# Kernel tuning notes

Measured on AMD Instinct MI355X. Metric: run time of the kernel, lower is better.

Reference implementation:

```python
import jax, jax.numpy as jnp
import numpy as np

E = 1024      # embed_size
H = 16        # heads
D = E // H    # head_dim = 64
FF = 4 * E    # forward_expansion * embed_size
B = 2
S = 2048
LN_EPS = 1e-5


def setup_inputs() -> dict:
    key = jax.random.key(0)
    ks = jax.random.split(key, 16)
    sc = 0.02
    inp = {
        'value': jax.random.normal(ks[0], (B, S, E), jnp.float32),
        'key':   jax.random.normal(ks[1], (B, S, E), jnp.float32),
        'query': jax.random.normal(ks[2], (B, S, E), jnp.float32),
        # causal mask, broadcast over batch and heads; 0 => masked
        'mask': jnp.tril(jnp.ones((S, S), jnp.int32))[None, None],
        # fc_out: Linear(E, E)
        'Wo': jax.random.normal(ks[3], (E, E), jnp.float32) * sc,
        'bo': jnp.zeros((E,), jnp.float32),
        # pH gate: Linear(E, E)
        'Wg': jax.random.normal(ks[4], (E, E), jnp.float32) * sc,
        'bg': jnp.zeros((E,), jnp.float32),
        # LayerNorms
        'g1': jnp.ones((E,), jnp.float32), 'b1': jnp.zeros((E,), jnp.float32),
        'g2': jnp.ones((E,), jnp.float32), 'b2': jnp.zeros((E,), jnp.float32),
        # FFN
        'W1': jax.random.normal(ks[5], (E, FF), jnp.float32) * sc,
        'bf1': jnp.zeros((FF,), jnp.float32),
        'W2': jax.random.normal(ks[6], (FF, E), jnp.float32) * sc,
        'bf2': jnp.zeros((E,), jnp.float32),
    }
    return inp


def layer_norm(x, g, b):
    mu = jnp.mean(x, axis=-1, keepdims=True)
    var = jnp.mean(jnp.square(x - mu), axis=-1, keepdims=True)
    return (x - mu) * jax.lax.rsqrt(var + LN_EPS) * g + b


def reference(value, key, query, mask, Wo, bo, Wg, bg, g1, b1, g2, b2, W1, bf1, W2, bf2):
    N, seq_len, _ = query.shape
    # NOTE: original module defines per-head Linear(values/keys/queries) but never
    # applies them in forward; faithful reference omits them too.
    v = value.reshape(N, seq_len, H, D).transpose(0, 2, 1, 3)  # nhkd
    k = key.reshape(N, seq_len, H, D).transpose(0, 2, 1, 3)
    q = query.reshape(N, seq_len, H, D).transpose(0, 2, 1, 3)  # nhqd

    energy = jnp.einsum('nhqd,nhkd->nhqk', q, k)
    energy = jnp.where(mask == 0, jnp.float32(-1e20), energy)
    # faithful: mask applied BEFORE scaling by 1/sqrt(head_dim)
    attention = jax.nn.softmax(energy / jnp.sqrt(jnp.float32(D)), axis=-1)
    out = jnp.einsum('nhqk,nhkd->nhqd', attention, v)
    out = out.transpose(0, 2, 1, 3).reshape(N, seq_len, E)
    attn_output = out @ Wo + bo

    x_avg = jnp.mean(query, axis=1, keepdims=True)       # (N,1,E)
    gate = jax.nn.sigmoid(x_avg @ Wg + bg)               # (N,1,E)
    gated = gate * attn_output

    x = layer_norm(gated + query, g1, b1)                # dropout p=0 -> identity
    ff = jax.nn.gelu(x @ W1 + bf1, approximate=False) @ W2 + bf2
    out_final = layer_norm(ff + x, g2, b2)
    return out_final
```

## Files before the change

kernel.cpp:

```cpp
#include <hip/hip_runtime.h>
#include <hip/hip_bf16.h>

#define S_LEN 2048
#define EMB   1024
#define NH    16
#define HD    64
#define FF_DIM 4096
#define BATCH 2

typedef __attribute__((ext_vector_type(8))) short bf16x8;
typedef __attribute__((ext_vector_type(4))) float f32x4;

__device__ __forceinline__ short f2bf(float x) {
  __hip_bfloat16 h = (__hip_bfloat16)x;
  return *(short*)&h;
}
__device__ __forceinline__ bf16x8 pack8(float4 a, float4 b) {
  bf16x8 o;
  o[0] = f2bf(a.x); o[1] = f2bf(a.y); o[2] = f2bf(a.z); o[3] = f2bf(a.w);
  o[4] = f2bf(b.x); o[5] = f2bf(b.y); o[6] = f2bf(b.z); o[7] = f2bf(b.w);
  return o;
}

__device__ __forceinline__ void gl2lds16(const void* g, void* l) {
  __builtin_amdgcn_global_load_lds(
      (const __attribute__((address_space(1))) unsigned*)g,
      (__attribute__((address_space(3))) unsigned*)l, 16, 0, 0);
}

__device__ __forceinline__ void transpose_tile(
    const float* in, short* outS, int R, int C, int bx, int by, int t) {
  __shared__ short Ts[64][65];
  int cb = bx * 64, rb = by * 64;
  for (int idx = t; idx < 4096; idx += 256) {
    int r = idx >> 6, c = idx & 63;
    Ts[r][c] = f2bf(in[(size_t)(rb + r) * C + cb + c]);
  }
  __syncthreads();
  for (int idx = t; idx < 4096; idx += 256) {
    int oc = idx >> 6, orr = idx & 63;
    outS[(size_t)(cb + oc) * R + rb + orr] = Ts[orr][oc];
  }
}

__global__ __launch_bounds__(256) void transpose_all(
    const float* __restrict__ Wo, const float* __restrict__ W1,
    const float* __restrict__ W2, __hip_bfloat16* __restrict__ WoT,
    __hip_bfloat16* __restrict__ W1T, __hip_bfloat16* __restrict__ W2T) {
  int id = blockIdx.x, t = threadIdx.x;
  if (id < 256)        transpose_tile(Wo, (short*)WoT, EMB, EMB,    id & 15,          id >> 4,          t);
  else if (id < 1280)  transpose_tile(W1, (short*)W1T, EMB, FF_DIM, (id - 256) & 63,  (id - 256) >> 6,  t);
  else                 transpose_tile(W2, (short*)W2T, FF_DIM, EMB, (id - 1280) & 15, (id - 1280) >> 4, t);
}

__global__ __launch_bounds__(256) void zero_f32(float* __restrict__ p) {
  p[blockIdx.x * 256 + threadIdx.x] = 0.f;
}

__global__ __launch_bounds__(256) void xavg_partial(
    const float* __restrict__ Q, float* __restrict__ xavg) {
  int b = blockIdx.y;
  int s0 = blockIdx.x * 16;
  int t = threadIdx.x;
  const float* base = Q + ((size_t)b * S_LEN + s0) * EMB + 4 * t;
  float4 acc = {0.f, 0.f, 0.f, 0.f};
#pragma unroll 4
  for (int r = 0; r < 16; r++) {
    float4 v = *(const float4*)(base + (size_t)r * EMB);
    acc.x += v.x; acc.y += v.y; acc.z += v.z; acc.w += v.w;
  }
  float* dst = xavg + b * EMB + 4 * t;
  const float inv = 1.f / (float)S_LEN;
  atomicAdd(dst + 0, acc.x * inv);
  atomicAdd(dst + 1, acc.y * inv);
  atomicAdd(dst + 2, acc.z * inv);
  atomicAdd(dst + 3, acc.w * inv);
}

__global__ __launch_bounds__(256) void gate_kernel(
    const float* __restrict__ xavg, const float* __restrict__ Wg,
    const float* __restrict__ bg, float* __restrict__ gate) {
  __shared__ float red[4][64];
  int b = blockIdx.y;
  int nl = threadIdx.x & 63;
  int n = blockIdx.x * 64 + nl;
  int kg = threadIdx.x >> 6;
  const float* xa = xavg + b * EMB;
  float s = 0.f;
#pragma unroll 4
  for (int k = kg * 256; k < kg * 256 + 256; k++)
    s += xa[k] * Wg[(size_t)k * EMB + n];
  red[kg][nl] = s;
  __syncthreads();
  if (kg == 0) {
    float tot = red[0][nl] + red[1][nl] + red[2][nl] + red[3][nl] + bg[n];
    gate[b * EMB + n] = 1.f / (1.f + __expf(-tot));
  }
}

__global__ __launch_bounds__(256) void pack_kv(
    const float* __restrict__ Kg, const float* __restrict__ Vg,
    __hip_bfloat16* __restrict__ Kp, __hip_bfloat16* __restrict__ Vt) {
  __shared__ short Vs[64][72];
  int s0 = blockIdx.x * 64, h = blockIdx.y, b = blockIdx.z;
  int t = threadIdx.x, r = t >> 2, c = (t & 3) * 16;
  size_t gin = ((size_t)b * S_LEN + s0 + r) * EMB + h * HD + c;
  {
    float4 a0 = *(const float4*)(Kg + gin);
    float4 a1 = *(const float4*)(Kg + gin + 4);
    float4 a2 = *(const float4*)(Kg + gin + 8);
    float4 a3 = *(const float4*)(Kg + gin + 12);
    short* kp = (short*)Kp + (((size_t)b * NH + h) * S_LEN + s0 + r) * HD + c;
    *(bf16x8*)(kp)     = pack8(a0, a1);
    *(bf16x8*)(kp + 8) = pack8(a2, a3);
  }
  {
    float4 a0 = *(const float4*)(Vg + gin);
    float4 a1 = *(const float4*)(Vg + gin + 4);
    float4 a2 = *(const float4*)(Vg + gin + 8);
    float4 a3 = *(const float4*)(Vg + gin + 12);
    *(bf16x8*)&Vs[r][c]     = pack8(a0, a1);
    *(bf16x8*)&Vs[r][c + 8] = pack8(a2, a3);
  }
  __syncthreads();
  bf16x8 o0, o1;
#pragma unroll
  for (int j = 0; j < 8; j++) o0[j] = Vs[c + j][r];
#pragma unroll
  for (int j = 0; j < 8; j++) o1[j] = Vs[c + 8 + j][r];
  short* vp = (short*)Vt + (((size_t)b * NH + h) * HD + r) * S_LEN + s0 + c;
  *(bf16x8*)(vp)     = o0;
  *(bf16x8*)(vp + 8) = o1;
}

__global__ __launch_bounds__(256) void flash_attn_mfma(
    const float* __restrict__ Q, const __hip_bfloat16* __restrict__ Kp,
    const __hip_bfloat16* __restrict__ Vtb, __hip_bfloat16* __restrict__ O) {
  __shared__ short Ks[64][72];
  __shared__ short Vt[64][72];
  __shared__ short Ps[4][16][72];
  int t = threadIdx.x;
  int w = t >> 6, lane = t & 63, quad = lane >> 4, l15 = lane & 15;
  int j = blockIdx.x;
  int p = j & 255, g = j >> 8;
  int bh = p & 31, c_ = p >> 5;
  int qb = (g == 0) ? c_ : (g == 1) ? (15 - c_) : (g == 2) ? (16 + c_) : (31 - c_);
  int h = bh & 15, b = bh >> 4;
  size_t base = ((size_t)b * S_LEN) * EMB + h * HD;
  const short* kpb = (const short*)Kp + ((size_t)b * NH + h) * S_LEN * HD;
  const short* vtb = (const short*)Vtb + ((size_t)b * NH + h) * HD * S_LEN;

  bf16x8 qf[2];
  {
    const float* qrow = Q + base + (size_t)(qb * 64 + w * 16 + l15) * EMB;
#pragma unroll
    for (int kc = 0; kc < 2; kc++) {
      float4 a = *(const float4*)(qrow + kc * 32 + quad * 8);
      float4 c = *(const float4*)(qrow + kc * 32 + quad * 8 + 4);
      a.x *= 0.125f; a.y *= 0.125f; a.z *= 0.125f; a.w *= 0.125f;
      c.x *= 0.125f; c.y *= 0.125f; c.z *= 0.125f; c.w *= 0.125f;
      qf[kc] = pack8(a, c);
    }
  }

  f32x4 acc[4];
  float lsum[4];
  f32x4 zero = {0.f, 0.f, 0.f, 0.f};
#pragma unroll
  for (int n = 0; n < 4; n++) acc[n] = zero;
#pragma unroll
  for (int r = 0; r < 4; r++) lsum[r] = 0.f;

  int r0 = t >> 2, c0 = (t & 3) * 16;
  bf16x8 kf0, kf1, vf0, vf1;
  {
    const short* kr = kpb + (size_t)r0 * HD + c0;
    kf0 = *(const bf16x8*)(kr); kf1 = *(const bf16x8*)(kr + 8);
    const short* vr = vtb + (size_t)r0 * S_LEN + c0;
    vf0 = *(const bf16x8*)(vr); vf1 = *(const bf16x8*)(vr + 8);
  }

  for (int kt = 0; kt <= qb; kt++) {
    __syncthreads();
    *(bf16x8*)&Ks[r0][c0]     = kf0;
    *(bf16x8*)&Ks[r0][c0 + 8] = kf1;
    *(bf16x8*)&Vt[r0][c0]     = vf0;
    *(bf16x8*)&Vt[r0][c0 + 8] = vf1;
    __syncthreads();
    if (kt < qb) {
      const short* kr = kpb + (size_t)((kt + 1) * 64 + r0) * HD + c0;
      kf0 = *(const bf16x8*)(kr); kf1 = *(const bf16x8*)(kr + 8);
      const short* vr = vtb + (size_t)r0 * S_LEN + (kt + 1) * 64 + c0;
      vf0 = *(const bf16x8*)(vr); vf1 = *(const bf16x8*)(vr + 8);
    }

    f32x4 sc[4];
#pragma unroll
    for (int n = 0; n < 4; n++) sc[n] = zero;
#pragma unroll
    for (int n = 0; n < 4; n++)
#pragma unroll
      for (int kc = 0; kc < 2; kc++) {
        bf16x8 kf = *(const bf16x8*)&Ks[n * 16 + l15][kc * 32 + quad * 8];
        sc[n] = __builtin_amdgcn_mfma_f32_16x16x32_bf16(qf[kc], kf, sc[n], 0, 0, 0);
      }

    bool diag = (kt == qb);
#pragma unroll
    for (int r = 0; r < 4; r++) {
      float p0 = __expf(sc[0][r]);
      float p1 = __expf(sc[1][r]);
      float p2 = __expf(sc[2][r]);
      float p3 = __expf(sc[3][r]);
      if (diag) {
        int rowL = w * 16 + quad * 4 + r;
        if (l15      > rowL) p0 = 0.f;
        if (l15 + 16 > rowL) p1 = 0.f;
        if (l15 + 32 > rowL) p2 = 0.f;
        if (l15 + 48 > rowL) p3 = 0.f;
      }
      lsum[r] += (p0 + p1) + (p2 + p3);
      short* prow = &Ps[w][quad * 4 + r][l15];
      prow[0]  = f2bf(p0);
      prow[16] = f2bf(p1);
      prow[32] = f2bf(p2);
      prow[48] = f2bf(p3);
    }
    asm volatile("s_waitcnt lgkmcnt(0)" ::: "memory");

    bf16x8 pf0 = *(const bf16x8*)&Ps[w][l15][quad * 8];
    bf16x8 pf1 = *(const bf16x8*)&Ps[w][l15][32 + quad * 8];
#pragma unroll
    for (int n = 0; n < 4; n++) {
      bf16x8 vfa = *(const bf16x8*)&Vt[n * 16 + l15][quad * 8];
      acc[n] = __builtin_amdgcn_mfma_f32_16x16x32_bf16(pf0, vfa, acc[n], 0, 0, 0);
      bf16x8 vfb = *(const bf16x8*)&Vt[n * 16 + l15][32 + quad * 8];
      acc[n] = __builtin_amdgcn_mfma_f32_16x16x32_bf16(pf1, vfb, acc[n], 0, 0, 0);
    }
  }

#pragma unroll
  for (int r = 0; r < 4; r++) {
    float l = lsum[r];
#pragma unroll
    for (int off = 1; off < 16; off <<= 1) l += __shfl_xor(l, off);
    float invl = 1.f / l;
    size_t orow = base + (size_t)(qb * 64 + w * 16 + quad * 4 + r) * EMB;
#pragma unroll
    for (int n = 0; n < 4; n++)
      O[orow + n * 16 + l15] = (__hip_bfloat16)(acc[n][r] * invl);
  }
}

template <int MODE, int TM>
__global__ __launch_bounds__(256) void gemm_bt(
    const __hip_bfloat16* __restrict__ A, const __hip_bfloat16* __restrict__ BT,
    int K, int N, const float* __restrict__ bias,
    const float* __restrict__ gate, const float* __restrict__ residF,
    const __hip_bfloat16* __restrict__ residB,
    float* __restrict__ outF, __hip_bfloat16* __restrict__ outB) {
  constexpr int MI = TM / 32;
  __shared__ short As[TM][32];
  __shared__ short Bs[128][32];
  int t = threadIdx.x;
  int w = t >> 6, lane = t & 63, quad = lane >> 4, l15 = lane & 15;
  int wm = (w >> 1) * (TM / 2), wn = (w & 1) * 64;
  int mBase = blockIdx.y * TM, nBase = blockIdx.x * 128;
  f32x4 acc[MI][4];
  f32x4 zero = {0.f, 0.f, 0.f, 0.f};
#pragma unroll
  for (int i = 0; i < MI; i++)
#pragma unroll
    for (int j = 0; j < 4; j++) acc[i][j] = zero;
  const short* Ag = (const short*)A;
  const short* Bg = (const short*)BT;
  int w16 = w * 16;
  int lr = lane >> 2;
  int lc = (lane & 3) * 8;
  for (int kb = 0; kb < K; kb += 32) {
    gl2lds16(&Ag[(size_t)(mBase + w16 + lr) * K + kb + lc], &As[w16][0]);
    if (TM == 128)
      gl2lds16(&Ag[(size_t)(mBase + 64 + w16 + lr) * K + kb + lc], &As[64 + w16][0]);
    gl2lds16(&Bg[(size_t)(nBase + w16 + lr) * K + kb + lc],      &Bs[w16][0]);
    gl2lds16(&Bg[(size_t)(nBase + 64 + w16 + lr) * K + kb + lc], &Bs[64 + w16][0]);
    __syncthreads();
    bf16x8 af[MI], bfr[4];
#pragma unroll
    for (int mi = 0; mi < MI; mi++) af[mi] = *(const bf16x8*)&As[wm + mi * 16 + l15][quad * 8];
#pragma unroll
    for (int ni = 0; ni < 4; ni++) bfr[ni] = *(const bf16x8*)&Bs[wn + ni * 16 + l15][quad * 8];
#pragma unroll
    for (int mi = 0; mi < MI; mi++)
#pragma unroll
      for (int ni = 0; ni < 4; ni++)
        acc[mi][ni] = __builtin_amdgcn_mfma_f32_16x16x32_bf16(af[mi], bfr[ni], acc[mi][ni], 0, 0, 0);
    __syncthreads();
  }
#pragma unroll
  for (int mi = 0; mi < MI; mi++) {
#pragma unroll
    for (int r = 0; r < 4; r++) {
      int row = mBase + wm + mi * 16 + quad * 4 + r;
#pragma unroll
      for (int ni = 0; ni < 4; ni++) {
        int col = nBase + wn + ni * 16 + l15;
        float v = acc[mi][ni][r];
        if (MODE == 0) {
          float g = gate[(row >> 11) * EMB + col];
          v = g * (v + bias[col]) + residF[(size_t)row * N + col];
          outF[(size_t)row * N + col] = v;
        } else if (MODE == 1) {
          v += bias[col];
          v = 0.5f * v * (1.0f + erff(v * 0.70710678118654752f));
          outB[(size_t)row * N + col] = (__hip_bfloat16)v;
        } else {
          v += bias[col] + (float)residB[(size_t)row * N + col];
          outF[(size_t)row * N + col] = v;
        }
      }
    }
  }
}

__device__ __forceinline__ float block_sum_256(float v) {
  __shared__ float sb[4];
#pragma unroll
  for (int off = 32; off > 0; off >>= 1) v += __shfl_down(v, off);
  int w = threadIdx.x >> 6, ln = threadIdx.x & 63;
  if (ln == 0) sb[w] = v;
  __syncthreads();
  float r = sb[0] + sb[1] + sb[2] + sb[3];
  __syncthreads();
  return r;
}

template <bool TO_BF16>
__global__ __launch_bounds__(256) void ln_kernel(
    const float* __restrict__ y, const float* __restrict__ g,
    const float* __restrict__ b, __hip_bfloat16* __restrict__ outB,
    float* __restrict__ outF) {
  size_t row = blockIdx.x;
  const float* yr = y + row * EMB;
  float v[4];
#pragma unroll
  for (int i = 0; i < 4; i++) v[i] = yr[threadIdx.x + i * 256];
  float s = block_sum_256(v[0] + v[1] + v[2] + v[3]);
  float mu = s * (1.f / (float)EMB);
  float q = 0.f;
#pragma unroll
  for (int i = 0; i < 4; i++) { float d = v[i] - mu; q += d * d; }
  q = block_sum_256(q);
  float rs = rsqrtf(q * (1.f / (float)EMB) + 1e-5f);
#pragma unroll
  for (int i = 0; i < 4; i++) {
    int e = threadIdx.x + i * 256;
    float o = (v[i] - mu) * rs * g[e] + b[e];
    if (TO_BF16) outB[row * EMB + e] = (__hip_bfloat16)o;
    else         outF[row * EMB + e] = o;
  }
}

extern "C" void kernel_launch(void* const* d_in, const int* in_sizes, int n_in,
                              void* d_out, int out_size, void* d_ws, size_t ws_size,
                              hipStream_t stream) {
  const float* Val = (const float*)d_in[0];
  const float* Key = (const float*)d_in[1];
  const float* Qry = (const float*)d_in[2];
  const float* Wo  = (const float*)d_in[4];
  const float* bo  = (const float*)d_in[5];
  const float* Wg  = (const float*)d_in[6];
  const float* bg  = (const float*)d_in[7];
  const float* g1  = (const float*)d_in[8];
  const float* b1  = (const float*)d_in[9];
  const float* g2  = (const float*)d_in[10];
  const float* b2  = (const float*)d_in[11];
  const float* W1  = (const float*)d_in[12];
  const float* bf1 = (const float*)d_in[13];
  const float* W2  = (const float*)d_in[14];
  const float* bf2 = (const float*)d_in[15];
  float* out = (float*)d_out;

  char* ws = (char*)d_ws;
  size_t off = 0;
  auto alloc = [&](size_t bytes) {
    char* p = ws + off;
    off += (bytes + 255) & ~(size_t)255;
    return p;
  };
  const size_t MB = 1024 * 1024;
  bool bigws = ws_size >= 78 * MB;

  __hip_bfloat16* WoT = (__hip_bfloat16*)alloc((size_t)EMB * EMB * 2);
  __hip_bfloat16* W1T = (__hip_bfloat16*)alloc((size_t)EMB * FF_DIM * 2);
  __hip_bfloat16* W2T = (__hip_bfloat16*)alloc((size_t)EMB * FF_DIM * 2);
  size_t kvRegion = bigws ? (size_t)BATCH * S_LEN * FF_DIM * 2
                          : (size_t)S_LEN * FF_DIM * 2;
  char* kvBase = alloc(kvRegion);
  __hip_bfloat16* Kpk  = (__hip_bfloat16*)kvBase;
  __hip_bfloat16* Vtb  = (__hip_bfloat16*)(kvBase + 8 * MB);
  __hip_bfloat16* Hbuf = (__hip_bfloat16*)kvBase;
  __hip_bfloat16* attnO = (__hip_bfloat16*)alloc((size_t)BATCH * S_LEN * EMB * 2);
  float* ybuf = (float*)alloc((size_t)BATCH * S_LEN * EMB * 4);
  float* xavg = (float*)alloc(BATCH * EMB * 4);
  float* gate = (float*)alloc(BATCH * EMB * 4);
  __hip_bfloat16* xb = attnO;
  float* zbuf = ybuf;

  transpose_all<<<2304, 256, 0, stream>>>(Wo, W1, W2, WoT, W1T, W2T);
  zero_f32<<<BATCH * EMB / 256, 256, 0, stream>>>(xavg);
  xavg_partial<<<dim3(128, BATCH), 256, 0, stream>>>(Qry, xavg);
  gate_kernel<<<dim3(16, BATCH), 256, 0, stream>>>(xavg, Wg, bg, gate);
  pack_kv<<<dim3(32, NH, BATCH), 256, 0, stream>>>(Key, Val, Kpk, Vtb);
  flash_attn_mfma<<<1024, 256, 0, stream>>>(Qry, Kpk, Vtb, attnO);
  gemm_bt<0, 64><<<dim3(8, 64), 256, 0, stream>>>(attnO, WoT, EMB, EMB, bo, gate, Qry, nullptr, ybuf, nullptr);
  ln_kernel<true><<<4096, 256, 0, stream>>>(ybuf, g1, b1, xb, nullptr);
  if (bigws) {
    gemm_bt<1, 128><<<dim3(32, 32), 256, 0, stream>>>(xb, W1T, EMB, FF_DIM, bf1, nullptr, nullptr, nullptr, nullptr, Hbuf);
    gemm_bt<2, 64><<<dim3(8, 64), 256, 0, stream>>>(Hbuf, W2T, FF_DIM, EMB, bf2, nullptr, nullptr, xb, zbuf, nullptr);
  } else {
    for (int b = 0; b < BATCH; b++) {
      const __hip_bfloat16* xbb = xb + (size_t)b * S_LEN * EMB;
      gemm_bt<1, 128><<<dim3(32, 16), 256, 0, stream>>>(xbb, W1T, EMB, FF_DIM, bf1, nullptr, nullptr, nullptr, nullptr, Hbuf);
      gemm_bt<2, 64><<<dim3(8, 32), 256, 0, stream>>>(Hbuf, W2T, FF_DIM, EMB, bf2, nullptr, nullptr, xbb,
                                                      zbuf + (size_t)b * S_LEN * EMB, nullptr);
    }
  }
  ln_kernel<false><<<4096, 256, 0, stream>>>(zbuf, g2, b2, nullptr, out);
}
```

Baseline: 439.7 us.

## Double-buffer GEMM LDS tiles with 64-wide K steps and XOR swizzle

Restructures the bf16 GEMM main loop to use two LDS buffers, prefetching the next K tile while the current one feeds the MFMAs, and drops one barrier per iteration. The K step doubles to 64, and LDS columns are XOR-swizzled by row to avoid bank conflicts on fragment reads. MFMA blocks are wrapped in s_setprio to favour matrix issue. LDS use quadruples, which may lower occupancy, and the prefetch relies on async global-to-LDS loads finishing before the single barrier.

```diff
diff --git a/kernel.cpp b/kernel.cpp
--- a/kernel.cpp
+++ b/kernel.cpp
@@ -260,8 +260,9 @@
     const __hip_bfloat16* __restrict__ residB,
     float* __restrict__ outF, __hip_bfloat16* __restrict__ outB) {
   constexpr int MI = TM / 32;
-  __shared__ short As[TM][32];
-  __shared__ short Bs[128][32];
+  constexpr int AR = TM / 32;
+  __shared__ short As[2][TM][64];
+  __shared__ short Bs[2][128][64];
   int t = threadIdx.x;
   int w = t >> 6, lane = t & 63, quad = lane >> 4, l15 = lane & 15;
   int wm = (w >> 1) * (TM / 2), wn = (w & 1) * 64;
@@ -274,28 +275,59 @@
     for (int j = 0; j < 4; j++) acc[i][j] = zero;
   const short* Ag = (const short*)A;
   const short* Bg = (const short*)BT;
-  int w16 = w * 16;
-  int lr = lane >> 2;
-  int lc = (lane & 3) * 8;
-  for (int kb = 0; kb < K; kb += 32) {
-    gl2lds16(&Ag[(size_t)(mBase + w16 + lr) * K + kb + lc], &As[w16][0]);
-    if (TM == 128)
-      gl2lds16(&Ag[(size_t)(mBase + 64 + w16 + lr) * K + kb + lc], &As[64 + w16][0]);
-    gl2lds16(&Bg[(size_t)(nBase + w16 + lr) * K + kb + lc],      &Bs[w16][0]);
-    gl2lds16(&Bg[(size_t)(nBase + 64 + w16 + lr) * K + kb + lc], &Bs[64 + w16][0]);
+
+  int rl = t >> 3;
+  int sck = t & 7;
+  int wrow = w << 3;
+
+  auto stage = [&](int buf, int kt) {
+    int kb = kt << 6;
+#pragma unroll
+    for (int rd = 0; rd < AR; rd++) {
+      int R = (rd << 5) + rl;
+      gl2lds16(&Ag[(size_t)(mBase + R) * K + kb + ((sck ^ (R & 7)) << 3)],
+               &As[buf][(rd << 5) + wrow][0]);
+    }
+#pragma unroll
+    for (int rd = 0; rd < 4; rd++) {
+      int R = (rd << 5) + rl;
+      gl2lds16(&Bg[(size_t)(nBase + R) * K + kb + ((sck ^ (R & 7)) << 3)],
+               &Bs[buf][(rd << 5) + wrow][0]);
+    }
+  };
+
+  const int nt = K >> 6;
+  stage(0, 0);
+  __syncthreads();
+  int cur = 0;
+  for (int kt = 0; kt < nt; kt++) {
+    if (kt + 1 < nt) stage(cur ^ 1, kt + 1);
+#pragma unroll
+    for (int kh = 0; kh < 2; kh++) {
+      bf16x8 af[MI], bfr[4];
+      int dch = (kh << 2) + quad;
+#pragma unroll
+      for (int mi = 0; mi < MI; mi++) {
+        int R = wm + mi * 16 + l15;
+        af[mi] = *(const bf16x8*)&As[cur][R][(dch ^ (R & 7)) << 3];
+      }
+#pragma unroll
+      for (int ni = 0; ni < 4; ni++) {
+        int R = wn + ni * 16 + l15;
+        bfr[ni] = *(const bf16x8*)&Bs[cur][R][(dch ^ (R & 7)) << 3];
+      }
+      __builtin_amdgcn_s_setprio(1);
+#pragma unroll
+      for (int mi = 0; mi < MI; mi++)
+#pragma unroll
+        for (int ni = 0; ni < 4; ni++)
+          acc[mi][ni] = __builtin_amdgcn_mfma_f32_16x16x32_bf16(af[mi], bfr[ni], acc[mi][ni], 0, 0, 0);
+      __builtin_amdgcn_s_setprio(0);
+    }
     __syncthreads();
-    bf16x8 af[MI], bfr[4];
-#pragma unroll
-    for (int mi = 0; mi < MI; mi++) af[mi] = *(const bf16x8*)&As[wm + mi * 16 + l15][quad * 8];
-#pragma unroll
-    for (int ni = 0; ni < 4; ni++) bfr[ni] = *(const bf16x8*)&Bs[wn + ni * 16 + l15][quad * 8];
-#pragma unroll
-    for (int mi = 0; mi < MI; mi++)
-#pragma unroll
-      for (int ni = 0; ni < 4; ni++)
-        acc[mi][ni] = __builtin_amdgcn_mfma_f32_16x16x32_bf16(af[mi], bfr[ni], acc[mi][ni], 0, 0, 0);
-    __syncthreads();
-  }
+    cur ^= 1;
+  }
+
 #pragma unroll
   for (int mi = 0; mi < MI; mi++) {
 #pragma unroll
```

After: 414.3 us. 1.06x faster.
